# Kernel optimization log

Measured on AMD Instinct MI355X. Metric: run time of the kernel, lower is better.

The kernel has to match this reference:

```python
import jax, jax.numpy as jnp
import numpy as np

N = 16384   # nodes at current level
M = 8192    # nodes at next (coarser) level
E = 524288  # edges (avg degree 32)
D = 128     # in_feats == out_feats
LN_EPS = 1e-5


def setup_inputs() -> dict:
    key = jax.random.key(0)
    ks = jax.random.split(key, 10)
    curr_h = jax.random.normal(ks[0], (N, D), jnp.float32)
    next_h = jax.random.normal(ks[1], (M, D), jnp.float32)
    curr_inc = jax.random.uniform(ks[2], (N, M), jnp.float32)
    edge_src = jax.random.randint(ks[3], (E,), 0, N, jnp.int32)
    edge_dst = jax.random.randint(ks[4], (E,), 0, N, jnp.int32)
    Wc = jax.random.normal(ks[5], (D, D), jnp.float32) / np.float32(np.sqrt(D))
    Wf = jax.random.normal(ks[6], (D, D), jnp.float32) / np.float32(np.sqrt(D))
    bc = jnp.zeros((D,), jnp.float32)
    bf = jnp.zeros((D,), jnp.float32)
    conv_w = jax.random.uniform(ks[7], (D,), jnp.float32)
    topDown_w = jax.random.uniform(ks[8], (D,), jnp.float32)
    gamma = jnp.ones((D,), jnp.float32)
    beta = jnp.zeros((D,), jnp.float32)
    return dict(curr_h=curr_h, next_h=next_h, curr_inc=curr_inc,
                Wc=Wc, bc=bc, Wf=Wf, bf=bf, conv_w=conv_w,
                topDown_w=topDown_w, gamma=gamma, beta=beta,
                edge_src=edge_src, edge_dst=edge_dst)


def _graph_conv(x, W, b, src, dst, n):
    # DGL GraphConv, norm='both', on graph with self-loops added.
    ones = jnp.ones(src.shape[0], x.dtype)
    out_deg = jax.ops.segment_sum(ones, src, num_segments=n) + 1.0  # +1 self-loop
    in_deg = jax.ops.segment_sum(ones, dst, num_segments=n) + 1.0
    xn = x * jax.lax.rsqrt(out_deg)[:, None]
    # neighbor SpMM + self-loop contribution
    agg = jax.ops.segment_sum(xn[src], dst, num_segments=n) + xn
    agg = agg * jax.lax.rsqrt(in_deg)[:, None]
    return agg @ W + b


def reference(curr_h, next_h, curr_inc, Wc, bc, Wf, bf, conv_w,
              topDown_w, gamma, beta, edge_src, edge_dst):
    n = curr_h.shape[0]
    conv_layer = _graph_conv(curr_h, Wc, bc, edge_src, edge_dst, n) * conv_w[None, :]
    fused_in = curr_inc @ next_h  # dense incidence matmul [N, D]
    top_down = _graph_conv(fused_in, Wf, bf, edge_src, edge_dst, n) * topDown_w[None, :]
    res = (conv_layer + top_down) * 0.5  # update == 'MEAN' over stack of 2
    # LayerNorm over feature dim
    mu = jnp.mean(res, axis=-1, keepdims=True)
    var = jnp.mean(jnp.square(res - mu), axis=-1, keepdims=True)
    res = (res - mu) * jax.lax.rsqrt(var + LN_EPS) * gamma + beta
    res = jax.nn.relu(res)  # activation == 'RELU'
    # dropout: eval mode -> identity
    return res
```

## Files before the change

kernel.cpp:

```cpp
#include <hip/hip_runtime.h>

constexpr int Nn = 16384;
constexpr int Mm = 8192;
constexpr int Ee = 524288;
constexpr int Dd = 128;

typedef __attribute__((ext_vector_type(8))) short short8v;
typedef __attribute__((ext_vector_type(4))) short short4v;
typedef __attribute__((ext_vector_type(4))) float float4v;

static __device__ __forceinline__ short f2bf(float f) {
    unsigned u = __builtin_bit_cast(unsigned, f);
    u += 0x7fffu + ((u >> 16) & 1u);
    return (short)(u >> 16);
}

__global__ void k_zero_i(int* __restrict__ p, int n) {
    int i = blockIdx.x * 256 + threadIdx.x;
    if (i < n) p[i] = 0;
}

__global__ void k_deg_count(const int* __restrict__ src, const int* __restrict__ dst,
                            int* __restrict__ cnt_out, int* __restrict__ cnt_in) {
    int e = blockIdx.x * 256 + threadIdx.x;
    if (e < Ee) {
        atomicAdd(&cnt_out[src[e]], 1);
        atomicAdd(&cnt_in[dst[e]], 1);
    }
}

__global__ void k_deg_fin(const int* __restrict__ cnt_out, const int* __restrict__ cnt_in,
                          float* __restrict__ rs_out, float* __restrict__ rs_in) {
    int i = blockIdx.x * 256 + threadIdx.x;
    if (i < Nn) {
        rs_out[i] = rsqrtf((float)(cnt_out[i] + 1));
        rs_in[i]  = rsqrtf((float)(cnt_in[i] + 1));
    }
}

__global__ void k_scan(const int* __restrict__ cnt, int* __restrict__ row_start) {
    __shared__ int s[1024];
    int t = threadIdx.x;
    int base = t * 16;
    int local[16];
    int sum = 0;
#pragma unroll
    for (int i = 0; i < 16; i++) { local[i] = cnt[base + i]; sum += local[i]; }
    s[t] = sum;
    __syncthreads();
    for (int off = 1; off < 1024; off <<= 1) {
        int v = (t >= off) ? s[t - off] : 0;
        __syncthreads();
        s[t] += v;
        __syncthreads();
    }
    int run = s[t] - sum;
#pragma unroll
    for (int i = 0; i < 16; i++) { row_start[base + i] = run; run += local[i]; }
    if (t == 1023) row_start[16384] = s[1023];
}

__global__ void k_fill(const int* __restrict__ src, const int* __restrict__ dst,
                       const int* __restrict__ row_start, int* __restrict__ cursor,
                       int* __restrict__ ebuf) {
    int e = blockIdx.x * 256 + threadIdx.x;
    if (e < Ee) {
        int d = dst[e];
        int pos = atomicAdd(&cursor[d], 1);
        ebuf[row_start[d] + pos] = src[e];
    }
}

__global__ void k_agg(const float* __restrict__ x, const float* __restrict__ rs_o,
                      const float* __restrict__ rs_i, const int* __restrict__ row_start,
                      const int* __restrict__ ebuf, float* __restrict__ agg) {
    int d = blockIdx.x * 4 + (threadIdx.x >> 6);
    int lane = threadIdx.x & 63;
    int c = lane * 2;
    int beg = row_start[d], end = row_start[d + 1];
    float ax = 0.f, ay = 0.f;
    int i = beg;
    for (; i + 1 < end; i += 2) {
        int s0 = ebuf[i], s1 = ebuf[i + 1];
        float r0 = rs_o[s0], r1 = rs_o[s1];
        float2 v0 = *(const float2*)(x + (size_t)s0 * 128 + c);
        float2 v1 = *(const float2*)(x + (size_t)s1 * 128 + c);
        ax += v0.x * r0 + v1.x * r1;
        ay += v0.y * r0 + v1.y * r1;
    }
    if (i < end) {
        int s0 = ebuf[i];
        float r0 = rs_o[s0];
        float2 v0 = *(const float2*)(x + (size_t)s0 * 128 + c);
        ax += v0.x * r0;
        ay += v0.y * r0;
    }
    float2 vs = *(const float2*)(x + (size_t)d * 128 + c);
    float ro = rs_o[d], ri = rs_i[d];
    float2 o;
    o.x = (ax + vs.x * ro) * ri;
    o.y = (ay + vs.y * ro) * ri;
    *(float2*)(agg + (size_t)d * 128 + c) = o;
}

__global__ void k_bt(const float* __restrict__ B, short* __restrict__ Bt) {
    __shared__ short T[32][40];
    int kt = blockIdx.x & 255;
    int nt = blockIdx.x >> 8;
    int t = threadIdx.x;
    int r = t >> 3;
    int c4 = (t & 7) * 4;
    float4 v = *(const float4*)(B + (size_t)(kt * 32 + r) * 128 + nt * 32 + c4);
    T[c4 + 0][r] = f2bf(v.x);
    T[c4 + 1][r] = f2bf(v.y);
    T[c4 + 2][r] = f2bf(v.z);
    T[c4 + 3][r] = f2bf(v.w);
    __syncthreads();
    int nl = t >> 3, ks = (t & 7) * 4;
    *(short4v*)(Bt + (size_t)(nt * 32 + nl) * 8192 + kt * 32 + ks) =
        *(const short4v*)(&T[nl][ks]);
}

__launch_bounds__(256, 2)
__global__ void k_mfma_gemm(const float* __restrict__ A, const short* __restrict__ Bt,
                            float* __restrict__ C) {
    __shared__ short As[32 * 72];
    __shared__ short Bs[128 * 72];

    const int tid = threadIdx.x;
    const int lane = tid & 63;
    const int wv = tid >> 6;
    const int row0 = blockIdx.x * 32;

    const int ar = tid >> 3;
    const int ak = (tid & 7) * 8;
    const float* Ap = A + (size_t)(row0 + ar) * Mm + ak;

    const int bn = tid >> 1;
    const int bk = (tid & 1) * 32;
    const short* Bp = Bt + (size_t)bn * Mm + bk;

    const int fm = lane & 15;
    const int fk = (lane >> 4) * 8;

    float4v acc[2][2] = {};

    for (int k0 = 0; k0 < Mm; k0 += 64) {
        float4 a0 = *(const float4*)(Ap + k0);
        float4 a1 = *(const float4*)(Ap + k0 + 4);
        short8v b0 = *(const short8v*)(Bp + k0);
        short8v b1 = *(const short8v*)(Bp + k0 + 8);
        short8v b2 = *(const short8v*)(Bp + k0 + 16);
        short8v b3 = *(const short8v*)(Bp + k0 + 24);
        __syncthreads();
        short8v ap;
        ap[0] = f2bf(a0.x); ap[1] = f2bf(a0.y); ap[2] = f2bf(a0.z); ap[3] = f2bf(a0.w);
        ap[4] = f2bf(a1.x); ap[5] = f2bf(a1.y); ap[6] = f2bf(a1.z); ap[7] = f2bf(a1.w);
        *(short8v*)(&As[ar * 72 + ak]) = ap;
        *(short8v*)(&Bs[bn * 72 + bk +  0]) = b0;
        *(short8v*)(&Bs[bn * 72 + bk +  8]) = b1;
        *(short8v*)(&Bs[bn * 72 + bk + 16]) = b2;
        *(short8v*)(&Bs[bn * 72 + bk + 24]) = b3;
        __syncthreads();
#pragma unroll
        for (int ks = 0; ks < 2; ks++) {
            const int kk = ks * 32 + fk;
            short8v a0f = *(const short8v*)(&As[fm * 72 + kk]);
            short8v a1f = *(const short8v*)(&As[(16 + fm) * 72 + kk]);
            short8v b0f = *(const short8v*)(&Bs[(wv * 32 + fm) * 72 + kk]);
            short8v b1f = *(const short8v*)(&Bs[(wv * 32 + 16 + fm) * 72 + kk]);
            acc[0][0] = __builtin_amdgcn_mfma_f32_16x16x32_bf16(a0f, b0f, acc[0][0], 0, 0, 0);
            acc[0][1] = __builtin_amdgcn_mfma_f32_16x16x32_bf16(a0f, b1f, acc[0][1], 0, 0, 0);
            acc[1][0] = __builtin_amdgcn_mfma_f32_16x16x32_bf16(a1f, b0f, acc[1][0], 0, 0, 0);
            acc[1][1] = __builtin_amdgcn_mfma_f32_16x16x32_bf16(a1f, b1f, acc[1][1], 0, 0, 0);
        }
    }

    const int crow = (lane >> 4) * 4;
#pragma unroll
    for (int mt = 0; mt < 2; mt++)
#pragma unroll
        for (int nt = 0; nt < 2; nt++)
#pragma unroll
            for (int r = 0; r < 4; r++)
                C[(size_t)(row0 + mt * 16 + crow + r) * 128 + wv * 32 + nt * 16 + fm] =
                    acc[mt][nt][r];
}

__launch_bounds__(256, 2)
__global__ void k_gemm(const float* __restrict__ A, const float* __restrict__ B,
                       float* __restrict__ C, int K,
                       const float* __restrict__ bias, const float* __restrict__ scale,
                       const float* __restrict__ prev, int mode) {
    __shared__ float As[32 * 36];
    __shared__ float Bs[32 * 128];

    const int tid = threadIdx.x;
    const int tx = tid & 31;
    const int ty = tid >> 5;
    const int c4 = tx * 4;
    const int r0 = ty * 4;
    const int row0 = blockIdx.x * 32;

    const int ar = tid >> 3;
    const int ak = (tid & 7) * 4;
    const float* Arow = A + (size_t)(row0 + ar) * K + ak;

    float acc[4][4] = {};

    for (int k0 = 0; k0 < K; k0 += 32) {
        float4 av = *(const float4*)(Arow + k0);
        float4 bv[4];
#pragma unroll
        for (int t = 0; t < 4; t++) {
            int idx = tid + t * 256;
            int br = idx >> 5, bc = (idx & 31) * 4;
            bv[t] = *(const float4*)(B + (size_t)(k0 + br) * 128 + bc);
        }
        __syncthreads();
        As[(ak + 0) * 36 + ar] = av.x;
        As[(ak + 1) * 36 + ar] = av.y;
        As[(ak + 2) * 36 + ar] = av.z;
        As[(ak + 3) * 36 + ar] = av.w;
#pragma unroll
        for (int t = 0; t < 4; t++) {
            int idx = tid + t * 256;
            int br = idx >> 5, bc = (idx & 31) * 4;
            *(float4*)(Bs + br * 128 + bc) = bv[t];
        }
        __syncthreads();
#pragma unroll
        for (int kk = 0; kk < 32; kk++) {
            float4 a4 = *(const float4*)(As + kk * 36 + r0);
            float4 b4 = *(const float4*)(Bs + kk * 128 + c4);
            float a[4] = {a4.x, a4.y, a4.z, a4.w};
            float b[4] = {b4.x, b4.y, b4.z, b4.w};
#pragma unroll
            for (int i = 0; i < 4; i++)
#pragma unroll
                for (int j = 0; j < 4; j++)
                    acc[i][j] = fmaf(a[i], b[j], acc[i][j]);
        }
    }

    float4 bi = *(const float4*)(bias + c4);
    float4 sc = *(const float4*)(scale + c4);
#pragma unroll
    for (int i = 0; i < 4; i++) {
        size_t o = (size_t)(row0 + r0 + i) * 128 + c4;
        float4 v = {acc[i][0], acc[i][1], acc[i][2], acc[i][3]};
        v.x = (v.x + bi.x) * sc.x;
        v.y = (v.y + bi.y) * sc.y;
        v.z = (v.z + bi.z) * sc.z;
        v.w = (v.w + bi.w) * sc.w;
        if (mode == 2) {
            float4 p = *(const float4*)(prev + o);
            v.x = (v.x + p.x) * 0.5f;
            v.y = (v.y + p.y) * 0.5f;
            v.z = (v.z + p.z) * 0.5f;
            v.w = (v.w + p.w) * 0.5f;
        }
        *(float4*)(C + o) = v;
    }
}

__global__ void k_ln_relu(const float* __restrict__ x, const float* __restrict__ gamma,
                          const float* __restrict__ beta, float* __restrict__ out) {
    int wave = threadIdx.x >> 6;
    int lane = threadIdx.x & 63;
    int row = blockIdx.x * 4 + wave;
    const float* xr = x + (size_t)row * 128;
    float2 v = *(const float2*)(xr + lane * 2);
    float s1 = v.x + v.y;
    float s2 = v.x * v.x + v.y * v.y;
#pragma unroll
    for (int m = 32; m >= 1; m >>= 1) {
        s1 += __shfl_xor(s1, m);
        s2 += __shfl_xor(s2, m);
    }
    float mu = s1 * (1.0f / 128.0f);
    float var = s2 * (1.0f / 128.0f) - mu * mu;
    float inv = rsqrtf(var + 1e-5f);
    float2 g = *(const float2*)(gamma + lane * 2);
    float2 b = *(const float2*)(beta + lane * 2);
    float2 o;
    o.x = fmaxf((v.x - mu) * inv * g.x + b.x, 0.0f);
    o.y = fmaxf((v.y - mu) * inv * g.y + b.y, 0.0f);
    *(float2*)(out + (size_t)row * 128 + lane * 2) = o;
}

extern "C" void kernel_launch(void* const* d_in, const int* in_sizes, int n_in,
                              void* d_out, int out_size, void* d_ws, size_t ws_size,
                              hipStream_t stream) {
    const float* curr_h    = (const float*)d_in[0];
    const float* next_h    = (const float*)d_in[1];
    const float* curr_inc  = (const float*)d_in[2];
    const float* Wc        = (const float*)d_in[3];
    const float* bc        = (const float*)d_in[4];
    const float* Wf        = (const float*)d_in[5];
    const float* bf        = (const float*)d_in[6];
    const float* conv_w    = (const float*)d_in[7];
    const float* topDown_w = (const float*)d_in[8];
    const float* gamma     = (const float*)d_in[9];
    const float* beta      = (const float*)d_in[10];
    const int*   esrc      = (const int*)d_in[11];
    const int*   edst      = (const int*)d_in[12];
    float* out = (float*)d_out;

    char* w = (char*)d_ws;
    int*   cnt_out = (int*)w;    w += (size_t)Nn * 4;
    int*   cnt_in  = (int*)w;    w += (size_t)Nn * 4;
    int*   cursor  = (int*)w;    w += (size_t)Nn * 4;
    int*   row_st  = (int*)w;    w += (size_t)16388 * 4;
    int*   ebuf    = (int*)w;    w += (size_t)Ee * 4;
    float* rs_out  = (float*)w;  w += (size_t)Nn * 4;
    float* rs_in   = (float*)w;  w += (size_t)Nn * 4;
    short* Bt      = (short*)w;  w += (size_t)Dd * Mm * 2;
    float* fused   = (float*)w;  w += (size_t)Nn * Dd * 4;
    float* agg     = (float*)w;  w += (size_t)Nn * Dd * 4;
    float* path    = (float*)w;  w += (size_t)Nn * Dd * 4;

    k_zero_i<<<(3 * Nn + 255) / 256, 256, 0, stream>>>(cnt_out, 3 * Nn);
    k_deg_count<<<Ee / 256, 256, 0, stream>>>(esrc, edst, cnt_out, cnt_in);
    k_deg_fin<<<Nn / 256, 256, 0, stream>>>(cnt_out, cnt_in, rs_out, rs_in);
    k_scan<<<1, 1024, 0, stream>>>(cnt_in, row_st);
    k_fill<<<Ee / 256, 256, 0, stream>>>(esrc, edst, row_st, cursor, ebuf);

    k_bt<<<1024, 256, 0, stream>>>(next_h, Bt);
    k_mfma_gemm<<<Nn / 32, 256, 0, stream>>>(curr_inc, Bt, fused);

    k_agg<<<Nn / 4, 256, 0, stream>>>(curr_h, rs_out, rs_in, row_st, ebuf, agg);
    k_gemm<<<Nn / 32, 256, 0, stream>>>(agg, Wc, path, Dd, bc, conv_w, nullptr, 1);

    k_agg<<<Nn / 4, 256, 0, stream>>>(fused, rs_out, rs_in, row_st, ebuf, agg);
    k_gemm<<<Nn / 32, 256, 0, stream>>>(agg, Wf, path, Dd, bf, topDown_w, path, 2);

    k_ln_relu<<<Nn / 4, 256, 0, stream>>>(path, gamma, beta, out);
}
```

Baseline: 998.9 us.

## Fuse aggregation, both GraphConv GEMMs, mean and LayerNorm into one tail kernel

Merges the two neighbour-aggregation passes, the two 128x128 projections with bias and scale, the mean and the LayerNorm+ReLU into a single per-32-row-block kernel that keeps aggregated rows in shared memory. It also folds the zeroing into the transpose kernel and the degree rsqrt into the scan. This removes several intermediate N x 128 round trips through global memory and six kernel launches. In exchange, each block is larger, uses more shared memory and registers, and has fewer blocks (512), so latency hiding for the gather phase may suffer.

Result: no change. 1.006 ms (+0.7%).

```diff
diff --git a/kernel.cpp b/kernel.cpp
--- a/kernel.cpp
+++ b/kernel.cpp
@@ -15,98 +15,17 @@
     return (short)(u >> 16);
 }
 
-__global__ void k_zero_i(int* __restrict__ p, int n) {
-    int i = blockIdx.x * 256 + threadIdx.x;
-    if (i < n) p[i] = 0;
-}
-
-__global__ void k_deg_count(const int* __restrict__ src, const int* __restrict__ dst,
-                            int* __restrict__ cnt_out, int* __restrict__ cnt_in) {
-    int e = blockIdx.x * 256 + threadIdx.x;
-    if (e < Ee) {
-        atomicAdd(&cnt_out[src[e]], 1);
-        atomicAdd(&cnt_in[dst[e]], 1);
-    }
-}
-
-__global__ void k_deg_fin(const int* __restrict__ cnt_out, const int* __restrict__ cnt_in,
-                          float* __restrict__ rs_out, float* __restrict__ rs_in) {
-    int i = blockIdx.x * 256 + threadIdx.x;
-    if (i < Nn) {
-        rs_out[i] = rsqrtf((float)(cnt_out[i] + 1));
-        rs_in[i]  = rsqrtf((float)(cnt_in[i] + 1));
-    }
-}
-
-__global__ void k_scan(const int* __restrict__ cnt, int* __restrict__ row_start) {
-    __shared__ int s[1024];
-    int t = threadIdx.x;
-    int base = t * 16;
-    int local[16];
-    int sum = 0;
-#pragma unroll
-    for (int i = 0; i < 16; i++) { local[i] = cnt[base + i]; sum += local[i]; }
-    s[t] = sum;
-    __syncthreads();
-    for (int off = 1; off < 1024; off <<= 1) {
-        int v = (t >= off) ? s[t - off] : 0;
-        __syncthreads();
-        s[t] += v;
-        __syncthreads();
-    }
-    int run = s[t] - sum;
-#pragma unroll
-    for (int i = 0; i < 16; i++) { row_start[base + i] = run; run += local[i]; }
-    if (t == 1023) row_start[16384] = s[1023];
-}
-
-__global__ void k_fill(const int* __restrict__ src, const int* __restrict__ dst,
-                       const int* __restrict__ row_start, int* __restrict__ cursor,
-                       int* __restrict__ ebuf) {
-    int e = blockIdx.x * 256 + threadIdx.x;
-    if (e < Ee) {
-        int d = dst[e];
-        int pos = atomicAdd(&cursor[d], 1);
-        ebuf[row_start[d] + pos] = src[e];
-    }
-}
-
-__global__ void k_agg(const float* __restrict__ x, const float* __restrict__ rs_o,
-                      const float* __restrict__ rs_i, const int* __restrict__ row_start,
-                      const int* __restrict__ ebuf, float* __restrict__ agg) {
-    int d = blockIdx.x * 4 + (threadIdx.x >> 6);
-    int lane = threadIdx.x & 63;
-    int c = lane * 2;
-    int beg = row_start[d], end = row_start[d + 1];
-    float ax = 0.f, ay = 0.f;
-    int i = beg;
-    for (; i + 1 < end; i += 2) {
-        int s0 = ebuf[i], s1 = ebuf[i + 1];
-        float r0 = rs_o[s0], r1 = rs_o[s1];
-        float2 v0 = *(const float2*)(x + (size_t)s0 * 128 + c);
-        float2 v1 = *(const float2*)(x + (size_t)s1 * 128 + c);
-        ax += v0.x * r0 + v1.x * r1;
-        ay += v0.y * r0 + v1.y * r1;
-    }
-    if (i < end) {
-        int s0 = ebuf[i];
-        float r0 = rs_o[s0];
-        float2 v0 = *(const float2*)(x + (size_t)s0 * 128 + c);
-        ax += v0.x * r0;
-        ay += v0.y * r0;
-    }
-    float2 vs = *(const float2*)(x + (size_t)d * 128 + c);
-    float ro = rs_o[d], ri = rs_i[d];
-    float2 o;
-    o.x = (ax + vs.x * ro) * ri;
-    o.y = (ay + vs.y * ro) * ri;
-    *(float2*)(agg + (size_t)d * 128 + c) = o;
-}
-
-__global__ void k_bt(const float* __restrict__ B, short* __restrict__ Bt) {
+__global__ void k_bt_zero(const float* __restrict__ B, short* __restrict__ Bt,
+                          int* __restrict__ zp) {
+    int b = blockIdx.x;
+    if (b >= 1024) {
+        int i = (b - 1024) * 256 + threadIdx.x;
+        if (i < 3 * Nn) zp[i] = 0;
+        return;
+    }
     __shared__ short T[32][40];
-    int kt = blockIdx.x & 255;
-    int nt = blockIdx.x >> 8;
+    int kt = b & 255;
+    int nt = b >> 8;
     int t = threadIdx.x;
     int r = t >> 3;
     int c4 = (t & 7) * 4;
@@ -119,6 +38,56 @@
     int nl = t >> 3, ks = (t & 7) * 4;
     *(short4v*)(Bt + (size_t)(nt * 32 + nl) * 8192 + kt * 32 + ks) =
         *(const short4v*)(&T[nl][ks]);
+}
+
+__global__ void k_deg_count(const int* __restrict__ src, const int* __restrict__ dst,
+                            int* __restrict__ cnt_out, int* __restrict__ cnt_in) {
+    int e = blockIdx.x * 256 + threadIdx.x;
+    if (e < Ee) {
+        atomicAdd(&cnt_out[src[e]], 1);
+        atomicAdd(&cnt_in[dst[e]], 1);
+    }
+}
+
+__global__ void k_scan(const int* __restrict__ cnt_in, const int* __restrict__ cnt_out,
+                       int* __restrict__ row_start,
+                       float* __restrict__ rs_in, float* __restrict__ rs_out) {
+    __shared__ int s[1024];
+    int t = threadIdx.x;
+    int base = t * 16;
+    int local[16];
+    int sum = 0;
+#pragma unroll
+    for (int i = 0; i < 16; i++) {
+        int ci = cnt_in[base + i];
+        local[i] = ci;
+        sum += ci;
+        rs_in[base + i]  = rsqrtf((float)(ci + 1));
+        rs_out[base + i] = rsqrtf((float)(cnt_out[base + i] + 1));
+    }
+    s[t] = sum;
+    __syncthreads();
+    for (int off = 1; off < 1024; off <<= 1) {
+        int v = (t >= off) ? s[t - off] : 0;
+        __syncthreads();
+        s[t] += v;
+        __syncthreads();
+    }
+    int run = s[t] - sum;
+#pragma unroll
+    for (int i = 0; i < 16; i++) { row_start[base + i] = run; run += local[i]; }
+    if (t == 1023) row_start[16384] = s[1023];
+}
+
+__global__ void k_fill(const int* __restrict__ src, const int* __restrict__ dst,
+                       const int* __restrict__ row_start, int* __restrict__ cursor,
+                       int* __restrict__ ebuf) {
+    int e = blockIdx.x * 256 + threadIdx.x;
+    if (e < Ee) {
+        int d = dst[e];
+        int pos = atomicAdd(&cursor[d], 1);
+        ebuf[row_start[d] + pos] = src[e];
+    }
 }
 
 __launch_bounds__(256, 2)
@@ -188,105 +157,139 @@
 }
 
 __launch_bounds__(256, 2)
-__global__ void k_gemm(const float* __restrict__ A, const float* __restrict__ B,
-                       float* __restrict__ C, int K,
-                       const float* __restrict__ bias, const float* __restrict__ scale,
-                       const float* __restrict__ prev, int mode) {
-    __shared__ float As[32 * 36];
-    __shared__ float Bs[32 * 128];
+__global__ void k_tail(const float* __restrict__ curr_h, const float* __restrict__ fused,
+                       const float* __restrict__ rs_o, const float* __restrict__ rs_i,
+                       const int* __restrict__ row_start, const int* __restrict__ ebuf,
+                       const float* __restrict__ Wc, const float* __restrict__ bc,
+                       const float* __restrict__ conv_w,
+                       const float* __restrict__ Wf, const float* __restrict__ bf,
+                       const float* __restrict__ tdw,
+                       const float* __restrict__ gamma, const float* __restrict__ beta,
+                       float* __restrict__ out) {
+    __shared__ float A1[32][132];
+    __shared__ float A2[32][132];
+    __shared__ float Bs[32][132];
 
     const int tid = threadIdx.x;
-    const int tx = tid & 31;
-    const int ty = tid >> 5;
-    const int c4 = tx * 4;
-    const int r0 = ty * 4;
+    const int lane = tid & 63;
+    const int wv = tid >> 6;
     const int row0 = blockIdx.x * 32;
-
-    const int ar = tid >> 3;
-    const int ak = (tid & 7) * 4;
-    const float* Arow = A + (size_t)(row0 + ar) * K + ak;
-
-    float acc[4][4] = {};
-
-    for (int k0 = 0; k0 < K; k0 += 32) {
-        float4 av = *(const float4*)(Arow + k0);
-        float4 bv[4];
-#pragma unroll
-        for (int t = 0; t < 4; t++) {
-            int idx = tid + t * 256;
-            int br = idx >> 5, bc = (idx & 31) * 4;
-            bv[t] = *(const float4*)(B + (size_t)(k0 + br) * 128 + bc);
-        }
-        __syncthreads();
-        As[(ak + 0) * 36 + ar] = av.x;
-        As[(ak + 1) * 36 + ar] = av.y;
-        As[(ak + 2) * 36 + ar] = av.z;
-        As[(ak + 3) * 36 + ar] = av.w;
-#pragma unroll
-        for (int t = 0; t < 4; t++) {
-            int idx = tid + t * 256;
-            int br = idx >> 5, bc = (idx & 31) * 4;
-            *(float4*)(Bs + br * 128 + bc) = bv[t];
-        }
-        __syncthreads();
-#pragma unroll
-        for (int kk = 0; kk < 32; kk++) {
-            float4 a4 = *(const float4*)(As + kk * 36 + r0);
-            float4 b4 = *(const float4*)(Bs + kk * 128 + c4);
-            float a[4] = {a4.x, a4.y, a4.z, a4.w};
-            float b[4] = {b4.x, b4.y, b4.z, b4.w};
-#pragma unroll
-            for (int i = 0; i < 4; i++)
-#pragma unroll
-                for (int j = 0; j < 4; j++)
-                    acc[i][j] = fmaf(a[i], b[j], acc[i][j]);
-        }
-    }
-
-    float4 bi = *(const float4*)(bias + c4);
-    float4 sc = *(const float4*)(scale + c4);
+    const int c = lane * 2;
+
+    for (int rr = 0; rr < 8; rr++) {
+        const int rl = wv * 8 + rr;
+        const int d = row0 + rl;
+        const int beg = row_start[d], end = row_start[d + 1];
+        float a1x = 0.f, a1y = 0.f, a2x = 0.f, a2y = 0.f;
+        int i = beg;
+        for (; i + 1 < end; i += 2) {
+            int s0 = ebuf[i], s1 = ebuf[i + 1];
+            float r0v = rs_o[s0], r1v = rs_o[s1];
+            float2 u0 = *(const float2*)(curr_h + (size_t)s0 * 128 + c);
+            float2 v0 = *(const float2*)(fused  + (size_t)s0 * 128 + c);
+            float2 u1 = *(const float2*)(curr_h + (size_t)s1 * 128 + c);
+            float2 v1 = *(const float2*)(fused  + (size_t)s1 * 128 + c);
+            a1x += u0.x * r0v + u1.x * r1v;
+            a1y += u0.y * r0v + u1.y * r1v;
+            a2x += v0.x * r0v + v1.x * r1v;
+            a2y += v0.y * r0v + v1.y * r1v;
+        }
+        if (i < end) {
+            int s0 = ebuf[i];
+            float r0v = rs_o[s0];
+            float2 u0 = *(const float2*)(curr_h + (size_t)s0 * 128 + c);
+            float2 v0 = *(const float2*)(fused  + (size_t)s0 * 128 + c);
+            a1x += u0.x * r0v; a1y += u0.y * r0v;
+            a2x += v0.x * r0v; a2y += v0.y * r0v;
+        }
+        float ro = rs_o[d], ri = rs_i[d];
+        float2 us = *(const float2*)(curr_h + (size_t)d * 128 + c);
+        float2 vs = *(const float2*)(fused  + (size_t)d * 128 + c);
+        *(float2*)(&A1[rl][c]) = float2{(a1x + us.x * ro) * ri, (a1y + us.y * ro) * ri};
+        *(float2*)(&A2[rl][c]) = float2{(a2x + vs.x * ro) * ri, (a2y + vs.y * ro) * ri};
+    }
+
+    const int tx = tid & 31, ty = tid >> 5;
+    const int c4 = tx * 4, r0 = ty * 4;
+    float acc[2][4][4] = {};
+
+#pragma unroll
+    for (int m = 0; m < 2; m++) {
+        const float* W = m ? Wf : Wc;
+        const float(*Asrc)[132] = m ? A2 : A1;
+        for (int k0 = 0; k0 < 128; k0 += 32) {
+            float4 bv[4];
+#pragma unroll
+            for (int t4 = 0; t4 < 4; t4++) {
+                int idx = tid + t4 * 256;
+                bv[t4] = *(const float4*)(W + (size_t)(k0 + (idx >> 5)) * 128 + (idx & 31) * 4);
+            }
+            __syncthreads();
+#pragma unroll
+            for (int t4 = 0; t4 < 4; t4++) {
+                int idx = tid + t4 * 256;
+                *(float4*)(&Bs[idx >> 5][(idx & 31) * 4]) = bv[t4];
+            }
+            __syncthreads();
+#pragma unroll
+            for (int kq = 0; kq < 8; kq++) {
+                float4 a4[4];
+#pragma unroll
+                for (int i = 0; i < 4; i++)
+                    a4[i] = *(const float4*)(&Asrc[r0 + i][k0 + kq * 4]);
+#pragma unroll
+                for (int q = 0; q < 4; q++) {
+                    float4 b4 = *(const float4*)(&Bs[kq * 4 + q][c4]);
+#pragma unroll
+                    for (int i = 0; i < 4; i++) {
+                        float av = ((const float*)&a4[i])[q];
+                        acc[m][i][0] = fmaf(av, b4.x, acc[m][i][0]);
+                        acc[m][i][1] = fmaf(av, b4.y, acc[m][i][1]);
+                        acc[m][i][2] = fmaf(av, b4.z, acc[m][i][2]);
+                        acc[m][i][3] = fmaf(av, b4.w, acc[m][i][3]);
+                    }
+                }
+            }
+        }
+    }
+
+    const float4 bcv = *(const float4*)(bc + c4);
+    const float4 cwv = *(const float4*)(conv_w + c4);
+    const float4 bfv = *(const float4*)(bf + c4);
+    const float4 twv = *(const float4*)(tdw + c4);
+    const float4 gv  = *(const float4*)(gamma + c4);
+    const float4 bev = *(const float4*)(beta + c4);
+
+    float res[4][4];
 #pragma unroll
     for (int i = 0; i < 4; i++) {
-        size_t o = (size_t)(row0 + r0 + i) * 128 + c4;
-        float4 v = {acc[i][0], acc[i][1], acc[i][2], acc[i][3]};
-        v.x = (v.x + bi.x) * sc.x;
-        v.y = (v.y + bi.y) * sc.y;
-        v.z = (v.z + bi.z) * sc.z;
-        v.w = (v.w + bi.w) * sc.w;
-        if (mode == 2) {
-            float4 p = *(const float4*)(prev + o);
-            v.x = (v.x + p.x) * 0.5f;
-            v.y = (v.y + p.y) * 0.5f;
-            v.z = (v.z + p.z) * 0.5f;
-            v.w = (v.w + p.w) * 0.5f;
-        }
-        *(float4*)(C + o) = v;
-    }
-}
-
-__global__ void k_ln_relu(const float* __restrict__ x, const float* __restrict__ gamma,
-                          const float* __restrict__ beta, float* __restrict__ out) {
-    int wave = threadIdx.x >> 6;
-    int lane = threadIdx.x & 63;
-    int row = blockIdx.x * 4 + wave;
-    const float* xr = x + (size_t)row * 128;
-    float2 v = *(const float2*)(xr + lane * 2);
-    float s1 = v.x + v.y;
-    float s2 = v.x * v.x + v.y * v.y;
-#pragma unroll
-    for (int m = 32; m >= 1; m >>= 1) {
-        s1 += __shfl_xor(s1, m);
-        s2 += __shfl_xor(s2, m);
-    }
-    float mu = s1 * (1.0f / 128.0f);
-    float var = s2 * (1.0f / 128.0f) - mu * mu;
-    float inv = rsqrtf(var + 1e-5f);
-    float2 g = *(const float2*)(gamma + lane * 2);
-    float2 b = *(const float2*)(beta + lane * 2);
-    float2 o;
-    o.x = fmaxf((v.x - mu) * inv * g.x + b.x, 0.0f);
-    o.y = fmaxf((v.y - mu) * inv * g.y + b.y, 0.0f);
-    *(float2*)(out + (size_t)row * 128 + lane * 2) = o;
+#pragma unroll
+        for (int j = 0; j < 4; j++) {
+            float p1 = (acc[0][i][j] + ((const float*)&bcv)[j]) * ((const float*)&cwv)[j];
+            float p2 = (acc[1][i][j] + ((const float*)&bfv)[j]) * ((const float*)&twv)[j];
+            res[i][j] = (p1 + p2) * 0.5f;
+        }
+    }
+#pragma unroll
+    for (int i = 0; i < 4; i++) {
+        float s1 = res[i][0] + res[i][1] + res[i][2] + res[i][3];
+        float s2 = res[i][0] * res[i][0] + res[i][1] * res[i][1] +
+                   res[i][2] * res[i][2] + res[i][3] * res[i][3];
+#pragma unroll
+        for (int msk = 16; msk >= 1; msk >>= 1) {
+            s1 += __shfl_xor(s1, msk);
+            s2 += __shfl_xor(s2, msk);
+        }
+        float mu = s1 * (1.0f / 128.0f);
+        float var = s2 * (1.0f / 128.0f) - mu * mu;
+        float inv = rsqrtf(var + 1e-5f);
+        float4 o;
+        o.x = fmaxf((res[i][0] - mu) * inv * gv.x + bev.x, 0.0f);
+        o.y = fmaxf((res[i][1] - mu) * inv * gv.y + bev.y, 0.0f);
+        o.z = fmaxf((res[i][2] - mu) * inv * gv.z + bev.z, 0.0f);
+        o.w = fmaxf((res[i][3] - mu) * inv * gv.w + bev.w, 0.0f);
+        *(float4*)(out + (size_t)(row0 + r0 + i) * 128 + c4) = o;
+    }
 }
 
 extern "C" void kernel_launch(void* const* d_in, const int* in_sizes, int n_in,
@@ -317,23 +320,13 @@
     float* rs_in   = (float*)w;  w += (size_t)Nn * 4;
     short* Bt      = (short*)w;  w += (size_t)Dd * Mm * 2;
     float* fused   = (float*)w;  w += (size_t)Nn * Dd * 4;
-    float* agg     = (float*)w;  w += (size_t)Nn * Dd * 4;
-    float* path    = (float*)w;  w += (size_t)Nn * Dd * 4;
-
-    k_zero_i<<<(3 * Nn + 255) / 256, 256, 0, stream>>>(cnt_out, 3 * Nn);
+
+    k_bt_zero<<<1024 + 192, 256, 0, stream>>>(next_h, Bt, cnt_out);
     k_deg_count<<<Ee / 256, 256, 0, stream>>>(esrc, edst, cnt_out, cnt_in);
-    k_deg_fin<<<Nn / 256, 256, 0, stream>>>(cnt_out, cnt_in, rs_out, rs_in);
-    k_scan<<<1, 1024, 0, stream>>>(cnt_in, row_st);
+    k_scan<<<1, 1024, 0, stream>>>(cnt_in, cnt_out, row_st, rs_in, rs_out);
     k_fill<<<Ee / 256, 256, 0, stream>>>(esrc, edst, row_st, cursor, ebuf);
-
-    k_bt<<<1024, 256, 0, stream>>>(next_h, Bt);
     k_mfma_gemm<<<Nn / 32, 256, 0, stream>>>(curr_inc, Bt, fused);
-
-    k_agg<<<Nn / 4, 256, 0, stream>>>(curr_h, rs_out, rs_in, row_st, ebuf, agg);
-    k_gemm<<<Nn / 32, 256, 0, stream>>>(agg, Wc, path, Dd, bc, conv_w, nullptr, 1);
-
-    k_agg<<<Nn / 4, 256, 0, stream>>>(fused, rs_out, rs_in, row_st, ebuf, agg);
-    k_gemm<<<Nn / 32, 256, 0, stream>>>(agg, Wf, path, Dd, bf, topDown_w, path, 2);
-
-    k_ln_relu<<<Nn / 4, 256, 0, stream>>>(path, gamma, beta, out);
-}
+    k_tail<<<Nn / 32, 256, 0, stream>>>(curr_h, fused, rs_out, rs_in, row_st, ebuf,
+                                        Wc, bc, conv_w, Wf, bf, topDown_w,
+                                        gamma, beta, out);
+}
```
